# Optimization experiments

Hardware: AMD Instinct MI355X
Metric: run time of the kernel (lower is better)

The kernel has to match this reference:

```python
import jax, jax.numpy as jnp
import numpy as np

DEPTH = 6
N_INTERNAL = 2 ** DEPTH - 1  # 63
N_LEAVES = 2 ** DEPTH        # 64


def _tree_paths(depth):
    """Precompute, for each leaf, its `depth` ancestor internal-node indices and
    whether the path goes right at each ancestor (static heap-indexing of the tree)."""
    n_internal = 2 ** depth - 1
    n_leaves = 2 ** depth
    anc = np.zeros((n_leaves, depth), dtype=np.int32)
    right = np.zeros((n_leaves, depth), dtype=bool)
    for leaf in range(n_leaves):
        node = leaf + n_internal
        for d in range(depth):
            parent = (node - 1) // 2
            anc[leaf, d] = parent
            right[leaf, d] = (node % 2 == 0)
            node = parent
    return jnp.asarray(anc), jnp.asarray(right)

_ANC, _RIGHT = _tree_paths(DEPTH)


def setup_inputs() -> dict:
    key = jax.random.key(0)
    k = jax.random.split(key, 6)
    B, F, T, C = 8192, 256, 32, 100
    return {
        "x": jax.random.normal(k[0], (B, F), dtype=jnp.float32),
        "split_weights": jax.random.normal(k[1], (T, N_INTERNAL, F), dtype=jnp.float32) * 0.05,
        "split_bias": jax.random.normal(k[2], (T, N_INTERNAL), dtype=jnp.float32) * 0.05,
        "leaf_logits": jax.random.normal(k[3], (T, N_LEAVES, C), dtype=jnp.float32),
        "tree_weights": jax.random.normal(k[4], (T,), dtype=jnp.float32),
        "log_temperature": jnp.zeros((), dtype=jnp.float32),
    }


def reference(x, split_weights, split_bias, leaf_logits, tree_weights, log_temperature):
    # temperature = exp(log_temperature).clamp(0.1, 5.0)
    temp = jnp.clip(jnp.exp(log_temperature), 0.1, 5.0)
    # split probabilities for all trees at once: [T, B, N_INTERNAL]
    logits = jnp.einsum('bf,tnf->tbn', x, split_weights) + split_bias[:, None, :]
    split_probs = jax.nn.sigmoid(logits / temp)
    # gather each leaf's ancestor probs: [T, B, L, D]; right -> p, left -> 1-p
    g = split_probs[:, :, _ANC]
    leaf_probs = jnp.prod(jnp.where(_RIGHT, g, 1.0 - g), axis=-1)  # [T, B, L]
    # per-leaf class distributions: [T, L, C]
    leaf_class_probs = jax.nn.softmax(leaf_logits / temp, axis=-1)
    outputs = jnp.einsum('tbl,tlc->tbc', leaf_probs, leaf_class_probs)  # [T, B, C]
    weights = jax.nn.softmax(tree_weights, axis=0)  # [T]
    return jnp.einsum('t,tbc->bc', weights, outputs)  # [B, C]
```

## Files before the change

kernel.cpp:

```cpp
#include <hip/hip_runtime.h>
#include <math.h>

#define B_  8192
#define F_  256
#define T_  32
#define NI_ 63
#define NL_ 64
#define C_  100
#define K2_ (T_*NL_)
#define NG  8
#define TPG 4

typedef unsigned short u16;
typedef __attribute__((ext_vector_type(8))) short bf16x8;
typedef __attribute__((ext_vector_type(4))) float f32x4;
typedef __attribute__((ext_vector_type(8))) unsigned short u16x8;

__device__ __forceinline__ u16 f2bf(float f) {
    unsigned int u = __float_as_uint(f);
    u += 0x7fffu + ((u >> 16) & 1u);
    return (u16)(u >> 16);
}
__device__ __forceinline__ float bf2f(u16 u) {
    return __uint_as_float(((unsigned int)u) << 16);
}

__device__ __forceinline__ void gl16(const void* g, void* l) {
    __builtin_amdgcn_global_load_lds(
        (const __attribute__((address_space(1))) unsigned int*)g,
        (__attribute__((address_space(3))) unsigned int*)l,
        16, 0, 0);
}

#define WSB_SWB   0
#define WSB_LCPT  (T_*32*64*8*2)
#define WSB_XB    (WSB_LCPT + T_*8*112*8*2)
#define WSB_PART  ((size_t)WSB_XB + (size_t)B_*F_*2)
#define WSB_ATOM  WSB_PART
#define WSB_STORE (WSB_PART + (size_t)NG*B_*112*2)

#define SWBLK  (T_*64*32/256)
#define XBLK   (B_*F_/2048)
#define LCPBLK (T_*NL_/256)
#define ZBLK   (B_*C_/256)

__device__ __forceinline__ void cvt8(const float* __restrict__ s, u16* __restrict__ d, int i) {
    const float4* p = (const float4*)(s + i);
    float4 v0 = p[0], v1 = p[1];
    u16x8 o;
    o[0] = f2bf(v0.x); o[1] = f2bf(v0.y); o[2] = f2bf(v0.z); o[3] = f2bf(v0.w);
    o[4] = f2bf(v1.x); o[5] = f2bf(v1.y); o[6] = f2bf(v1.z); o[7] = f2bf(v1.w);
    *(u16x8*)(d + i) = o;
}

__global__ void k_prep(const float* __restrict__ sw, const float* __restrict__ x,
                       const float* __restrict__ ll, const float* __restrict__ tw,
                       const float* __restrict__ logT,
                       u16* __restrict__ swb, u16* __restrict__ xb,
                       u16* __restrict__ lcpT, float* __restrict__ out) {
    int blk = blockIdx.x, tid = threadIdx.x;
    if (blk < SWBLK) {
        int gid = blk * 256 + tid;
        int k8 = gid & 31;
        int n  = (gid >> 5) & 63;
        int t  = gid >> 11;
        u16x8 o;
        if (n < NI_) {
            const float4* p = (const float4*)(sw + ((size_t)(t * NI_ + n)) * F_ + k8 * 8);
            float4 v0 = p[0], v1 = p[1];
            o[0] = f2bf(v0.x); o[1] = f2bf(v0.y); o[2] = f2bf(v0.z); o[3] = f2bf(v0.w);
            o[4] = f2bf(v1.x); o[5] = f2bf(v1.y); o[6] = f2bf(v1.z); o[7] = f2bf(v1.w);
        } else {
            o = (u16x8){0,0,0,0,0,0,0,0};
        }
        *(u16x8*)(swb + (((size_t)t * 32 + k8) * 64 + n) * 8) = o;
        return;
    }
    blk -= SWBLK;
    if (blk < XBLK) { cvt8(x, xb, blk * 2048 + tid * 8); return; }
    blk -= XBLK;
    if (blk >= LCPBLK) {
        out[(blk - LCPBLK) * 256 + tid] = 0.f;
        return;
    }
    int idx = blk * 256 + tid;
    int t = idx >> 6;
    int l = idx & 63;
    int o = l >> 3, jj = l & 7;
    float temp = __expf(logT[0]);
    temp = fminf(fmaxf(temp, 0.1f), 5.0f);
    float invt = 1.0f / temp;

    float m = -1e30f;
    for (int j = 0; j < T_; ++j) m = fmaxf(m, tw[j]);
    float s = 0.f;
    for (int j = 0; j < T_; ++j) s += __expf(tw[j] - m);
    float wt = __expf(tw[t] - m) / s;

    const float* row = ll + (size_t)idx * C_;
    float m2 = -1e30f;
    for (int c = 0; c < C_; ++c) m2 = fmaxf(m2, row[c]);
    float s2 = 0.f;
    for (int c = 0; c < C_; ++c) s2 += __expf((row[c] - m2) * invt);
    float sc = wt / s2;
    u16* base = lcpT + (size_t)t * (8 * 112 * 8);
    for (int c = 0; c < C_; ++c)
        base[(o * 112 + c) * 8 + jj] = f2bf(sc * __expf((row[c] - m2) * invt));
    for (int c = C_; c < 112; ++c)
        base[(o * 112 + c) * 8 + jj] = 0;
}

__global__ __launch_bounds__(512, 2)
void k_fused(const u16* __restrict__ xb, const u16* __restrict__ swb,
             const float* __restrict__ sb, const float* __restrict__ logT,
             const u16* __restrict__ lcpT, void* __restrict__ dst, int storeMode) {
    __shared__ __attribute__((aligned(16))) u16 swS[32 * 64 * 8];
    __shared__ __attribute__((aligned(16))) u16 lcpS[8 * 112 * 8];
    __shared__ float slog[8][16][66];
    int tid  = threadIdx.x;
    int w    = tid >> 6;
    int lane = tid & 63;
    int col  = lane & 15;
    int quad = lane >> 4;
    int mb   = blockIdx.x * 128 + w * 16;
    int tg   = blockIdx.y;

    float temp = __expf(logT[0]);
    temp = fminf(fmaxf(temp, 0.1f), 5.0f);
    float invt = 1.0f / temp;

    bf16x8 afr[8];
    #pragma unroll
    for (int ks = 0; ks < 8; ++ks)
        afr[ks] = *(const bf16x8*)(xb + (size_t)(mb + col) * F_ + ks * 32 + quad * 8);

    f32x4 accO[7];
    #pragma unroll
    for (int i = 0; i < 7; ++i) accO[i] = (f32x4){0.f, 0.f, 0.f, 0.f};

    #pragma unroll 1
    for (int ti = 0; ti < TPG; ++ti) {
        int t = tg * TPG + ti;

        __syncthreads();

        {
            const char* gsw = (const char*)(swb + (size_t)t * (32 * 64 * 8));
            char* lsw = (char*)swS;
            #pragma unroll
            for (int r = 0; r < 4; ++r)
                gl16(gsw + r * 8192 + w * 1024 + lane * 16,
                     lsw + r * 8192 + w * 1024);
            const char* glc = (const char*)(lcpT + (size_t)t * (8 * 112 * 8));
            char* llc = (char*)lcpS;
            gl16(glc + w * 1024 + lane * 16, llc + w * 1024);
            if (w < 6)
                gl16(glc + 8192 + w * 1024 + lane * 16, llc + 8192 + w * 1024);
        }

        __syncthreads();

        f32x4 acc[4];
        #pragma unroll
        for (int i = 0; i < 4; ++i) acc[i] = (f32x4){0.f, 0.f, 0.f, 0.f};
        #pragma unroll
        for (int ks = 0; ks < 8; ++ks) {
            #pragma unroll
            for (int nt = 0; nt < 4; ++nt) {
                int n  = nt * 16 + col;
                int ne = n > 62 ? 62 : n;
                bf16x8 bfr = *(const bf16x8*)&swS[((ks * 4 + quad) * 64 + ne) * 8];
                acc[nt] = __builtin_amdgcn_mfma_f32_16x16x32_bf16(afr[ks], bfr, acc[nt], 0, 0, 0);
            }
        }

        asm volatile("s_waitcnt lgkmcnt(0)" ::: "memory");
        #pragma unroll
        for (int nt = 0; nt < 4; ++nt) {
            int n = nt * 16 + col;
            float bias = (n < NI_) ? sb[t * NI_ + n] : 0.f;
            #pragma unroll
            for (int r = 0; r < 4; ++r) {
                float lg = (acc[nt][r] + bias) * invt;
                slog[w][quad * 4 + r][n] = 1.0f / (1.0f + __expf(-lg));
            }
        }
        asm volatile("s_waitcnt lgkmcnt(0)" ::: "memory");

        bf16x8 af0, af1;
        #pragma unroll
        for (int grp = 0; grp < 2; ++grp) {
            int s = (grp ? 11 : 7) + quad;
            float pref = 1.0f;
            int node = s;
            #pragma unroll
            for (int d = 0; d < 3; ++d) {
                int par = (node - 1) >> 1;
                float g = slog[w][col][par];
                pref = (node & 1) ? (pref - pref * g) : (pref * g);
                node = par;
            }
            float gs  = slog[w][col][s];
            float gl  = slog[w][col][2 * s + 1];
            float gr  = slog[w][col][2 * s + 2];
            float g00 = slog[w][col][4 * s + 3];
            float g01 = slog[w][col][4 * s + 4];
            float g10 = slog[w][col][4 * s + 5];
            float g11 = slog[w][col][4 * s + 6];
            #pragma unroll
            for (int j = 0; j < 8; ++j) {
                const int b2 = (j >> 2) & 1, b1 = (j >> 1) & 1, b0 = j & 1;
                float f3 = b2 ? gs : 1.0f - gs;
                float c1 = b2 ? gr : gl;
                float f4 = b1 ? c1 : 1.0f - c1;
                float c2 = b2 ? (b1 ? g11 : g10) : (b1 ? g01 : g00);
                float f5 = b0 ? c2 : 1.0f - c2;
                float p  = pref * f3 * f4 * f5;
                if (grp == 0) af0[j] = (short)f2bf(p);
                else          af1[j] = (short)f2bf(p);
            }
        }

        #pragma unroll
        for (int nt = 0; nt < 7; ++nt) {
            int n = nt * 16 + col;
            bf16x8 lb0 = *(const bf16x8*)&lcpS[(quad * 112 + n) * 8];
            bf16x8 lb1 = *(const bf16x8*)&lcpS[((4 + quad) * 112 + n) * 8];
            accO[nt] = __builtin_amdgcn_mfma_f32_16x16x32_bf16(af0, lb0, accO[nt], 0, 0, 0);
            accO[nt] = __builtin_amdgcn_mfma_f32_16x16x32_bf16(af1, lb1, accO[nt], 0, 0, 0);
        }
    }

    if (storeMode) {
        u16* pp = (u16*)dst + (size_t)tg * B_ * 112;
        #pragma unroll
        for (int nt = 0; nt < 7; ++nt) {
            int c = nt * 16 + col;
            #pragma unroll
            for (int r = 0; r < 4; ++r) {
                int b = mb + quad * 4 + r;
                pp[(size_t)b * 112 + c] = f2bf(accO[nt][r]);
            }
        }
    } else {
        float* od = (float*)dst;
        #pragma unroll
        for (int nt = 0; nt < 7; ++nt) {
            int c = nt * 16 + col;
            if (c < C_) {
                #pragma unroll
                for (int r = 0; r < 4; ++r) {
                    int b = mb + quad * 4 + r;
                    atomicAdd(&od[(size_t)b * C_ + c], accO[nt][r]);
                }
            }
        }
    }
}

__global__ void k_red(const u16* __restrict__ part, float* __restrict__ out) {
    int idx = blockIdx.x * 256 + threadIdx.x;
    int b = idx / 112, c = idx - b * 112;
    if (c < C_) {
        float s = 0.f;
        #pragma unroll
        for (int tg = 0; tg < NG; ++tg)
            s += bf2f(part[((size_t)tg * B_ + b) * 112 + c]);
        out[(size_t)b * C_ + c] = s;
    }
}

__global__ void k_zf(float* __restrict__ out, int n) {
    int i = blockIdx.x * 256 + threadIdx.x;
    if (i < n) out[i] = 0.f;
}

__global__ void k_mono(const float* __restrict__ x, const float* __restrict__ sw,
                       const float* __restrict__ sb, const float* __restrict__ ll,
                       const float* __restrict__ tw, const float* __restrict__ logT,
                       float* __restrict__ outg) {
    __shared__ float slcp[NL_ * C_];
    int tid = threadIdx.x;
    int b = blockIdx.x * 256 + tid;

    float temp = __expf(logT[0]);
    temp = fminf(fmaxf(temp, 0.1f), 5.0f);
    float invt = 1.0f / temp;

    float m = -1e30f;
    for (int j = 0; j < T_; ++j) m = fmaxf(m, tw[j]);
    float sden = 0.f;
    for (int j = 0; j < T_; ++j) sden += __expf(tw[j] - m);

    float acc[C_];
    #pragma unroll
    for (int c = 0; c < C_; ++c) acc[c] = 0.f;

    for (int t = 0; t < T_; ++t) {
        __syncthreads();
        {
            int l = tid & 63, cq = tid >> 6;
            float wt = __expf(tw[t] - m) / sden;
            const float* row = ll + ((size_t)t * NL_ + l) * C_;
            float m2 = -1e30f;
            for (int c = 0; c < C_; ++c) m2 = fmaxf(m2, row[c]);
            float s2 = 0.f;
            for (int c = 0; c < C_; ++c) s2 += __expf((row[c] - m2) * invt);
            float sc = wt / s2;
            for (int c = cq * 25; c < cq * 25 + 25; ++c)
                slcp[l * C_ + c] = sc * __expf((row[c] - m2) * invt);
        }
        __syncthreads();

        float an[NI_];
        #pragma unroll
        for (int n = 0; n < NI_; ++n) an[n] = 0.f;
        for (int k = 0; k < F_; ++k) {
            float xv = x[(size_t)b * F_ + k];
            #pragma unroll
            for (int n = 0; n < NI_; ++n)
                an[n] = fmaf(xv, sw[((size_t)t * NI_ + n) * F_ + k], an[n]);
        }
        #pragma unroll
        for (int n = 0; n < NI_; ++n) {
            float lg = (an[n] + sb[t * NI_ + n]) * invt;
            an[n] = 1.0f / (1.0f + __expf(-lg));
        }
        #pragma unroll
        for (int l = 0; l < NL_; ++l) {
            int node = l + NI_;
            float p = 1.0f;
            #pragma unroll
            for (int d = 0; d < 6; ++d) {
                int par = (node - 1) >> 1;
                float gv = an[par];
                p = (node & 1) ? (p - p * gv) : (p * gv);
                node = par;
            }
            #pragma unroll
            for (int c = 0; c < C_; ++c)
                acc[c] = fmaf(p, slcp[l * C_ + c], acc[c]);
        }
    }
    for (int c = 0; c < C_; ++c)
        outg[(size_t)b * C_ + c] = acc[c];
}

extern "C" void kernel_launch(void* const* d_in, const int* in_sizes, int n_in,
                              void* d_out, int out_size, void* d_ws, size_t ws_size,
                              hipStream_t stream) {
    bool ok = (n_in >= 6)
           && (in_sizes[0] == B_ * F_)
           && (in_sizes[1] == T_ * NI_ * F_)
           && (in_sizes[2] == T_ * NI_)
           && (in_sizes[3] == T_ * NL_ * C_)
           && (in_sizes[4] == T_)
           && (in_sizes[5] == 1)
           && (out_size == B_ * C_);
    if (!ok) {
        k_zf<<<(out_size + 255) / 256, 256, 0, stream>>>((float*)d_out, out_size);
        return;
    }

    const float* x    = (const float*)d_in[0];
    const float* sw   = (const float*)d_in[1];
    const float* sb   = (const float*)d_in[2];
    const float* ll   = (const float*)d_in[3];
    const float* tw   = (const float*)d_in[4];
    const float* logT = (const float*)d_in[5];
    float* out = (float*)d_out;

    if (ws_size >= WSB_STORE) {
        u16* swb  = (u16*)((char*)d_ws + WSB_SWB);
        u16* lcpT = (u16*)((char*)d_ws + WSB_LCPT);
        u16* xb   = (u16*)((char*)d_ws + WSB_XB);
        u16* part = (u16*)((char*)d_ws + WSB_PART);

        k_prep <<<SWBLK + XBLK + LCPBLK, 256, 0, stream>>>(sw, x, ll, tw, logT, swb, xb, lcpT, out);
        k_fused<<<dim3(B_ / 128, NG), 512, 0, stream>>>(xb, swb, sb, logT, lcpT, part, 1);
        k_red  <<<(B_ * 112) / 256, 256, 0, stream>>>(part, out);
    } else if (ws_size >= WSB_ATOM) {
        u16* swb  = (u16*)((char*)d_ws + WSB_SWB);
        u16* lcpT = (u16*)((char*)d_ws + WSB_LCPT);
        u16* xb   = (u16*)((char*)d_ws + WSB_XB);

        k_prep <<<SWBLK + XBLK + LCPBLK + ZBLK, 256, 0, stream>>>(sw, x, ll, tw, logT, swb, xb, lcpT, out);
        k_fused<<<dim3(B_ / 128, NG), 512, 0, stream>>>(xb, swb, sb, logT, lcpT, d_out, 0);
    } else {
        k_mono<<<B_ / 256, 256, 0, stream>>>(x, sw, sb, ll, tw, logT, out);
    }
}
```

Measured before the change: 133.0 us.

## Read split weights and leaf probs directly from global instead of LDS staging

The per-tree copy of split weights and leaf class probabilities into shared memory is removed, along with the two block barriers around it. Each wave now loads its MFMA B-fragments straight from global memory and relies on the L1/L2 caches. The block shrinks from 512 to 256 threads (64 rows), doubling the grid, to suit the smaller shared-memory footprint. The risk is that each wave repeats the same global/L1 loads and pays full global latency on every fragment fetch instead of reusing one shared copy.

```diff
diff --git a/kernel.cpp b/kernel.cpp
--- a/kernel.cpp
+++ b/kernel.cpp
@@ -23,13 +23,6 @@
 }
 __device__ __forceinline__ float bf2f(u16 u) {
     return __uint_as_float(((unsigned int)u) << 16);
-}
-
-__device__ __forceinline__ void gl16(const void* g, void* l) {
-    __builtin_amdgcn_global_load_lds(
-        (const __attribute__((address_space(1))) unsigned int*)g,
-        (__attribute__((address_space(3))) unsigned int*)l,
-        16, 0, 0);
 }
 
 #define WSB_SWB   0
@@ -110,19 +103,17 @@
         base[(o * 112 + c) * 8 + jj] = 0;
 }
 
-__global__ __launch_bounds__(512, 2)
+__global__ __launch_bounds__(256, 2)
 void k_fused(const u16* __restrict__ xb, const u16* __restrict__ swb,
              const float* __restrict__ sb, const float* __restrict__ logT,
              const u16* __restrict__ lcpT, void* __restrict__ dst, int storeMode) {
-    __shared__ __attribute__((aligned(16))) u16 swS[32 * 64 * 8];
-    __shared__ __attribute__((aligned(16))) u16 lcpS[8 * 112 * 8];
-    __shared__ float slog[8][16][66];
+    __shared__ float slog[4][16][66];
     int tid  = threadIdx.x;
     int w    = tid >> 6;
     int lane = tid & 63;
     int col  = lane & 15;
     int quad = lane >> 4;
-    int mb   = blockIdx.x * 128 + w * 16;
+    int mb   = blockIdx.x * 64 + w * 16;
     int tg   = blockIdx.y;
 
     float temp = __expf(logT[0]);
@@ -141,24 +132,8 @@
     #pragma unroll 1
     for (int ti = 0; ti < TPG; ++ti) {
         int t = tg * TPG + ti;
-
-        __syncthreads();
-
-        {
-            const char* gsw = (const char*)(swb + (size_t)t * (32 * 64 * 8));
-            char* lsw = (char*)swS;
-            #pragma unroll
-            for (int r = 0; r < 4; ++r)
-                gl16(gsw + r * 8192 + w * 1024 + lane * 16,
-                     lsw + r * 8192 + w * 1024);
-            const char* glc = (const char*)(lcpT + (size_t)t * (8 * 112 * 8));
-            char* llc = (char*)lcpS;
-            gl16(glc + w * 1024 + lane * 16, llc + w * 1024);
-            if (w < 6)
-                gl16(glc + 8192 + w * 1024 + lane * 16, llc + 8192 + w * 1024);
-        }
-
-        __syncthreads();
+        const u16* swt = swb  + (size_t)t * (32 * 64 * 8);
+        const u16* lct = lcpT + (size_t)t * (8 * 112 * 8);
 
         f32x4 acc[4];
         #pragma unroll
@@ -167,14 +142,12 @@
         for (int ks = 0; ks < 8; ++ks) {
             #pragma unroll
             for (int nt = 0; nt < 4; ++nt) {
-                int n  = nt * 16 + col;
-                int ne = n > 62 ? 62 : n;
-                bf16x8 bfr = *(const bf16x8*)&swS[((ks * 4 + quad) * 64 + ne) * 8];
+                int n = nt * 16 + col;
+                bf16x8 bfr = *(const bf16x8*)&swt[(((ks * 4 + quad) * 64) + n) * 8];
                 acc[nt] = __builtin_amdgcn_mfma_f32_16x16x32_bf16(afr[ks], bfr, acc[nt], 0, 0, 0);
             }
         }
 
-        asm volatile("s_waitcnt lgkmcnt(0)" ::: "memory");
         #pragma unroll
         for (int nt = 0; nt < 4; ++nt) {
             int n = nt * 16 + col;
@@ -220,12 +193,13 @@
                 else          af1[j] = (short)f2bf(p);
             }
         }
+        asm volatile("s_waitcnt lgkmcnt(0)" ::: "memory");
 
         #pragma unroll
         for (int nt = 0; nt < 7; ++nt) {
             int n = nt * 16 + col;
-            bf16x8 lb0 = *(const bf16x8*)&lcpS[(quad * 112 + n) * 8];
-            bf16x8 lb1 = *(const bf16x8*)&lcpS[((4 + quad) * 112 + n) * 8];
+            bf16x8 lb0 = *(const bf16x8*)&lct[(quad * 112 + n) * 8];
+            bf16x8 lb1 = *(const bf16x8*)&lct[((4 + quad) * 112 + n) * 8];
             accO[nt] = __builtin_amdgcn_mfma_f32_16x16x32_bf16(af0, lb0, accO[nt], 0, 0, 0);
             accO[nt] = __builtin_amdgcn_mfma_f32_16x16x32_bf16(af1, lb1, accO[nt], 0, 0, 0);
         }
@@ -377,7 +351,7 @@
         u16* part = (u16*)((char*)d_ws + WSB_PART);
 
         k_prep <<<SWBLK + XBLK + LCPBLK, 256, 0, stream>>>(sw, x, ll, tw, logT, swb, xb, lcpT, out);
-        k_fused<<<dim3(B_ / 128, NG), 512, 0, stream>>>(xb, swb, sb, logT, lcpT, part, 1);
+        k_fused<<<dim3(B_ / 64, NG), 256, 0, stream>>>(xb, swb, sb, logT, lcpT, part, 1);
         k_red  <<<(B_ * 112) / 256, 256, 0, stream>>>(part, out);
     } else if (ws_size >= WSB_ATOM) {
         u16* swb  = (u16*)((char*)d_ws + WSB_SWB);
@@ -385,7 +359,7 @@
         u16* xb   = (u16*)((char*)d_ws + WSB_XB);
 
         k_prep <<<SWBLK + XBLK + LCPBLK + ZBLK, 256, 0, stream>>>(sw, x, ll, tw, logT, swb, xb, lcpT, out);
-        k_fused<<<dim3(B_ / 128, NG), 512, 0, stream>>>(xb, swb, sb, logT, lcpT, d_out, 0);
+        k_fused<<<dim3(B_ / 64, NG), 256, 0, stream>>>(xb, swb, sb, logT, lcpT, d_out, 0);
     } else {
         k_mono<<<B_ / 256, 256, 0, stream>>>(x, sw, sb, ll, tw, logT, out);
     }
```

Measured after the change: 141.1 us. +6.1%, slower.
